# Kernel tuning notes

Measured on AMD Instinct MI355X. Metric: run time of the kernel, lower is better.

## Reference

```python
import jax, jax.numpy as jnp
import numpy as np

N = 8192      # total QM atoms (concatenated over batch)
L = 6         # num_interactions / trajectory length
F = 256       # hidden_size
FH = F // 2
D_RBF = 32    # distance_embedding_size
E = 131072    # total probe edges
P = 32768     # total probes
CUTOFF = 4.0


def silu(x):
    return x * jax.nn.sigmoid(x)


def setup_inputs() -> dict:
    key = jax.random.key(0)
    ks = jax.random.split(key, 20)
    g = lambda k, shp, s=1.0: jax.random.normal(k, shp, dtype=jnp.float32) * s
    s_stack = g(ks[0], (N, L, F))
    v_stack = g(ks[1], (N, L, 3, F))
    # positions in a 2A box so all probe-atom distances < cutoff=4A
    atom_xyz = jax.random.uniform(ks[2], (N, 3), dtype=jnp.float32) * 2.0
    probe_xyz = jax.random.uniform(ks[3], (P, 3), dtype=jnp.float32) * 2.0
    cell = jnp.eye(3, dtype=jnp.float32) * 2.0
    probe_edges_displacement = jnp.zeros((E, 3), dtype=jnp.float32)
    atom_idx = jax.random.randint(ks[4], (E,), 0, N)
    probe_idx = jax.random.randint(ks[5], (E,), 0, P)
    probe_edges = jnp.stack([atom_idx, probe_idx], axis=1)
    in_dim = D_RBF + 3 * F  # e_pi || q_pi || n_i || S_JK
    return {
        's_stack': s_stack,
        'v_stack': v_stack,
        'atom_xyz': atom_xyz,
        'probe_xyz': probe_xyz,
        'cell': cell,
        'probe_edges_displacement': probe_edges_displacement,
        # JK attention MLP: F -> F/2 -> 1
        'attn_w1': g(ks[6], (F, FH), 1.0 / np.sqrt(F)),
        'attn_b1': jnp.zeros((FH,), jnp.float32),
        'attn_w2': g(ks[7], (FH, 1), 1.0 / np.sqrt(FH)),
        'attn_b2': jnp.zeros((1,), jnp.float32),
        # readout msg MLP: (D_rbf+3F) -> F -> F/2 -> 1
        'msg_w1': g(ks[8], (in_dim, F), 1.0 / np.sqrt(in_dim)),
        'msg_b1': jnp.zeros((F,), jnp.float32),
        'msg_w2': g(ks[9], (F, FH), 1.0 / np.sqrt(F)),
        'msg_b2': jnp.zeros((FH,), jnp.float32),
        'msg_w3': g(ks[10], (FH, 1), 1.0 / np.sqrt(FH)),
        'msg_b3': jnp.zeros((1,), jnp.float32),
        'probe_edges': probe_edges,
    }


def reference(s_stack, v_stack, atom_xyz, probe_xyz, cell, probe_edges_displacement,
              attn_w1, attn_b1, attn_w2, attn_b2,
              msg_w1, msg_b1, msg_w2, msg_b2, msg_w3, msg_b3,
              probe_edges):
    # ---- JKNetAggregation: node-level attention over layer trajectory ----
    h = silu(jnp.einsum('nlf,fh->nlh', s_stack, attn_w1) + attn_b1)   # [N,L,F/2]
    logits = (jnp.einsum('nlh,ho->nlo', h, attn_w2) + attn_b2)[..., 0]  # [N,L]
    a = jax.nn.softmax(logits, axis=1)                                  # [N,L]
    S_JK = jnp.einsum('nl,nlf->nf', a, s_stack)                         # [N,F]
    V_JK = jnp.einsum('nl,nlcf->ncf', a, v_stack)                       # [N,3,F]

    # ---- InfoBottleneckReadout: gather -> per-edge MLP -> scatter ----
    atom_idx = probe_edges[:, 0]
    probe_idx = probe_edges[:, 1]
    shift = probe_edges_displacement @ cell                             # [E,3] PBC shift
    diff = probe_xyz[probe_idx] - (atom_xyz[atom_idx] + shift)          # [E,3]
    dist = jnp.linalg.norm(diff, axis=-1)                               # [E]
    d = dist[:, None]
    n = jnp.arange(1, D_RBF + 1, dtype=jnp.float32)
    e_pi = jnp.sin(d * n * jnp.pi / CUTOFF) / (d + 1e-8)                # [E,D_rbf] sinc RBF
    r_hat = diff / (d + 1e-8)                                           # [E,3]
    V_e = V_JK[atom_idx]                                                # [E,3,F]
    q_pi = jnp.einsum('ecf,ec->ef', V_e, r_hat)                         # [E,F]
    n_i = jnp.linalg.norm(V_JK, axis=1)                                 # [N,F]
    h_pi = jnp.concatenate([e_pi, q_pi, n_i[atom_idx], S_JK[atom_idx]], axis=-1)  # [E,D_rbf+3F]
    m = silu(h_pi @ msg_w1 + msg_b1)
    m = silu(m @ msg_w2 + msg_b2)
    m = (m @ msg_w3 + msg_b3)[:, 0]                                     # [E]
    cw = jnp.where(dist < CUTOFF, 0.5 * (jnp.cos(jnp.pi * dist / CUTOFF) + 1.0), 0.0)
    rho = jax.ops.segment_sum(m * cw, probe_idx, num_segments=P)        # [P]
    return rho
```

## Files before the change

kernel.cpp:

```cpp
#include <hip/hip_runtime.h>
#include <math.h>
#include <stdint.h>


#define L_DIM 6
#define F_DIM 256
#define FH_DIM 128
#define DRBF 32
#define CUTOFF_F 4.0f
#define PI_F 3.14159265358979323846f

using bf16x8 = __attribute__((ext_vector_type(8))) short;
using f32x4v = __attribute__((ext_vector_type(4))) float;

__device__ __forceinline__ float silu_f(float x){ return x / (1.f + __expf(-x)); }

__device__ __forceinline__ unsigned short f2bf(float f){
    uint32_t u = __float_as_uint(f);
    uint32_t r = (u + 0x7fffu + ((u >> 16) & 1u)) >> 16;
    return (unsigned short)r;
}

__global__ __launch_bounds__(256) void kPrep(
    const float* __restrict__ msg_w1, const float* __restrict__ msg_w2,
    const float* __restrict__ attn_w1,
    unsigned short* __restrict__ w1bt, unsigned short* __restrict__ w1cdt,
    unsigned short* __restrict__ w2t, unsigned short* __restrict__ wA1t,
    float* __restrict__ rho, int P, int* __restrict__ cntpos, int CN)
{
    int idx = blockIdx.x * 256 + threadIdx.x;
    if (idx < 65536){
        int k = idx >> 8, j = idx & 255;
        w1bt[(size_t)j * 256 + k] = f2bf(msg_w1[(size_t)(DRBF + k) * F_DIM + j]);
    } else if (idx < 196608){
        int i2 = idx - 65536;
        int k = i2 >> 8, j = i2 & 255;
        w1cdt[(size_t)j * 512 + k] = f2bf(msg_w1[(size_t)(DRBF + 256 + k) * F_DIM + j]);
    } else if (idx < 229376){
        int i3 = idx - 196608;
        int k = i3 >> 7, h = i3 & 127;
        w2t[(size_t)h * 256 + k] = f2bf(msg_w2[(size_t)k * FH_DIM + h]);
    } else if (idx < 262144){
        int i4 = idx - 229376;
        int j = i4 >> 8, k = i4 & 255;
        wA1t[(size_t)j * 256 + k] = f2bf(attn_w1[(size_t)k * FH_DIM + j]);
    } else if (idx < 262144 + 32768){
        int i5 = idx - 262144;
        if (i5 < P) rho[i5] = 0.f;
    } else {
        int i6 = idx - 262144 - 32768;
        if (i6 < CN) cntpos[i6] = 0;
    }
}

__global__ __launch_bounds__(256) void kAW(
    const float* __restrict__ s_stack, const float* __restrict__ v_stack,
    const unsigned short* __restrict__ wA1t,
    const float* __restrict__ attn_b1, const float* __restrict__ attn_w2,
    unsigned short* __restrict__ VJKb, unsigned short* __restrict__ NISb,
    const int* __restrict__ pe, int* __restrict__ cnt, int E, int N)
{
    __shared__ float part[4][48];
    __shared__ float aw_l[8][8];

    const int t  = threadIdx.x;
    const int l  = t & 63;
    const int w  = t >> 6;
    const int lm = l & 15, lq = l >> 4;

    bf16x8 bfr[2][8];
    #pragma unroll
    for (int nt2 = 0; nt2 < 2; nt2++){
        const int col = w*32 + nt2*16 + lm;
        #pragma unroll
        for (int kb = 0; kb < 8; kb++)
            bfr[nt2][kb] = *(const bf16x8*)(wA1t + (size_t)col * 256 + kb*32 + lq*8);
    }
    const float b1a = attn_b1[w*32 + lm];
    const float b1b = attn_b1[w*32 + 16 + lm];
    const float w2a = attn_w2[w*32 + lm];
    const float w2b = attn_w2[w*32 + 16 + lm];

    const int n0 = blockIdx.x * 8;
    const size_t rbase = (size_t)n0 * L_DIM;
    const size_t rmax  = (size_t)N * L_DIM - 1;

    #pragma unroll
    for (int mt = 0; mt < 3; mt++){
        const size_t r0 = rbase + mt * 16;
        bf16x8 af[8];
        #pragma unroll
        for (int kb = 0; kb < 8; kb++){
            size_t row = r0 + lm; if (row > rmax) row = rmax;
            const float* ap = s_stack + row * 256 + kb*32 + lq*8;
            float4 fa = *(const float4*)ap;
            float4 fb = *(const float4*)(ap + 4);
            bf16x8 v;
            v[0] = (short)f2bf(fa.x); v[1] = (short)f2bf(fa.y);
            v[2] = (short)f2bf(fa.z); v[3] = (short)f2bf(fa.w);
            v[4] = (short)f2bf(fb.x); v[5] = (short)f2bf(fb.y);
            v[6] = (short)f2bf(fb.z); v[7] = (short)f2bf(fb.w);
            af[kb] = v;
        }
        f32x4v a0 = {0.f,0.f,0.f,0.f}, a1 = {0.f,0.f,0.f,0.f};
        #pragma unroll
        for (int kb = 0; kb < 8; kb++){
            a0 = __builtin_amdgcn_mfma_f32_16x16x32_bf16(af[kb], bfr[0][kb], a0, 0, 0, 0);
            a1 = __builtin_amdgcn_mfma_f32_16x16x32_bf16(af[kb], bfr[1][kb], a1, 0, 0, 0);
        }
        #pragma unroll
        for (int r = 0; r < 4; r++){
            float p = silu_f(a0[r] + b1a) * w2a + silu_f(a1[r] + b1b) * w2b;
            #pragma unroll
            for (int m = 8; m >= 1; m >>= 1) p += __shfl_xor(p, m, 64);
            if (lm == 0) part[w][mt*16 + lq*4 + r] = p;
        }
    }
    __syncthreads();
    if (t < 48) part[0][t] = part[0][t] + part[1][t] + part[2][t] + part[3][t];
    __syncthreads();
    if (t < 8){
        float e[L_DIM]; float mx = -1e30f;
        #pragma unroll
        for (int l6 = 0; l6 < L_DIM; l6++) mx = fmaxf(mx, part[0][t*L_DIM + l6]);
        float s = 0.f;
        #pragma unroll
        for (int l6 = 0; l6 < L_DIM; l6++){ e[l6] = __expf(part[0][t*L_DIM + l6] - mx); s += e[l6]; }
        float inv = 1.f / s;
        #pragma unroll
        for (int l6 = 0; l6 < L_DIM; l6++) aw_l[t][l6] = e[l6] * inv;
    }
    __syncthreads();

    #pragma unroll
    for (int aa = 0; aa < 2; aa++){
        const int n = min(n0 + w*2 + aa, N - 1);
        float aw[L_DIM];
        #pragma unroll
        for (int l6 = 0; l6 < L_DIM; l6++) aw[l6] = aw_l[w*2 + aa][l6];

        const float* sp = s_stack + (size_t)n * (L_DIM * F_DIM) + l * 4;
        const float* vp = v_stack + (size_t)n * (L_DIM * 3 * F_DIM) + l * 4;
        float4 v0 = {0.f,0.f,0.f,0.f}, v1 = {0.f,0.f,0.f,0.f}, v2 = {0.f,0.f,0.f,0.f};
        float4 sj = {0.f,0.f,0.f,0.f};
        #pragma unroll
        for (int l6 = 0; l6 < L_DIM; l6++){
            const float a = aw[l6];
            float4 ss = *(const float4*)(sp + (size_t)l6 * F_DIM);
            float4 x0 = *(const float4*)(vp + (size_t)(l6*3+0) * F_DIM);
            float4 x1 = *(const float4*)(vp + (size_t)(l6*3+1) * F_DIM);
            float4 x2 = *(const float4*)(vp + (size_t)(l6*3+2) * F_DIM);
            v0.x = fmaf(a, x0.x, v0.x); v0.y = fmaf(a, x0.y, v0.y);
            v0.z = fmaf(a, x0.z, v0.z); v0.w = fmaf(a, x0.w, v0.w);
            v1.x = fmaf(a, x1.x, v1.x); v1.y = fmaf(a, x1.y, v1.y);
            v1.z = fmaf(a, x1.z, v1.z); v1.w = fmaf(a, x1.w, v1.w);
            v2.x = fmaf(a, x2.x, v2.x); v2.y = fmaf(a, x2.y, v2.y);
            v2.z = fmaf(a, x2.z, v2.z); v2.w = fmaf(a, x2.w, v2.w);
            sj.x = fmaf(a, ss.x, sj.x); sj.y = fmaf(a, ss.y, sj.y);
            sj.z = fmaf(a, ss.z, sj.z); sj.w = fmaf(a, ss.w, sj.w);
        }
        float4 ni;
        ni.x = sqrtf(v0.x*v0.x + v1.x*v1.x + v2.x*v2.x);
        ni.y = sqrtf(v0.y*v0.y + v1.y*v1.y + v2.y*v2.y);
        ni.z = sqrtf(v0.z*v0.z + v1.z*v1.z + v2.z*v2.z);
        ni.w = sqrtf(v0.w*v0.w + v1.w*v1.w + v2.w*v2.w);

        ushort4 o;
        o = (ushort4){f2bf(v0.x), f2bf(v0.y), f2bf(v0.z), f2bf(v0.w)};
        *(ushort4*)&VJKb[((size_t)n*3 + 0) * F_DIM + l*4] = o;
        o = (ushort4){f2bf(v1.x), f2bf(v1.y), f2bf(v1.z), f2bf(v1.w)};
        *(ushort4*)&VJKb[((size_t)n*3 + 1) * F_DIM + l*4] = o;
        o = (ushort4){f2bf(v2.x), f2bf(v2.y), f2bf(v2.z), f2bf(v2.w)};
        *(ushort4*)&VJKb[((size_t)n*3 + 2) * F_DIM + l*4] = o;
        o = (ushort4){f2bf(ni.x), f2bf(ni.y), f2bf(ni.z), f2bf(ni.w)};
        *(ushort4*)&NISb[(size_t)n * 512 + l*4] = o;
        o = (ushort4){f2bf(sj.x), f2bf(sj.y), f2bf(sj.z), f2bf(sj.w)};
        *(ushort4*)&NISb[(size_t)n * 512 + 256 + l*4] = o;
    }

    {
        int e = blockIdx.x * 128 + t;
        if (t < 128 && e < E) atomicAdd(&cnt[pe[(size_t)e*2]], 1);
    }
}

__global__ __launch_bounds__(256) void kA2(
    const unsigned short* __restrict__ VJKb, const unsigned short* __restrict__ w1bt,
    const unsigned short* __restrict__ NISb, const unsigned short* __restrict__ w1cdt,
    const float* __restrict__ msg_b1, float* __restrict__ UT4,
    const int* __restrict__ pe, const int* __restrict__ offs,
    int* __restrict__ pos, int* __restrict__ perm, int E,
    int gU, int gUT)
{
    const int t  = threadIdx.x;
    const int l  = t & 63;
    const int w  = t >> 6;
    const int lm = l & 15, lq = l >> 4;

    if ((int)blockIdx.x >= gUT){
        int e = (blockIdx.x - gUT) * 256 + t;
        if (e < E){
            int i = pe[(size_t)e*2];
            int slot = atomicAdd(&pos[i], 1);
            perm[offs[i] + slot] = e;
        }
        return;
    }

    if ((int)blockIdx.x < gU){
        bf16x8 bfr[4][8];
        #pragma unroll
        for (int ct = 0; ct < 4; ct++)
            #pragma unroll
            for (int kb = 0; kb < 8; kb++)
                bfr[ct][kb] = *(const bf16x8*)(w1bt + (size_t)(w*64 + ct*16 + lm) * 256 + kb*32 + lq*8);

        const int r00 = blockIdx.x * 128;
        #pragma unroll 1
        for (int mt = 0; mt < 8; mt++){
            const int r0 = r00 + mt * 16;
            bf16x8 af[8];
            #pragma unroll
            for (int kb = 0; kb < 8; kb++)
                af[kb] = *(const bf16x8*)(VJKb + (size_t)(r0 + lm) * 256 + kb*32 + lq*8);
            f32x4v acc[4];
            #pragma unroll
            for (int ct = 0; ct < 4; ct++) acc[ct] = (f32x4v){0.f,0.f,0.f,0.f};
            #pragma unroll
            for (int kb = 0; kb < 8; kb++)
                #pragma unroll
                for (int ct = 0; ct < 4; ct++)
                    acc[ct] = __builtin_amdgcn_mfma_f32_16x16x32_bf16(af[kb], bfr[ct][kb], acc[ct], 0, 0, 0);
            #pragma unroll
            for (int ct = 0; ct < 4; ct++){
                const int col = w*64 + ct*16 + lm;
                #pragma unroll
                for (int r = 0; r < 4; r++){
                    const int row = r0 + lq*4 + r;
                    const int n = row / 3, c = row - n*3;
                    UT4[(((size_t)n << 8) + col) * 4 + c] = acc[ct][r];
                }
            }
        }
    } else {
        const int bid = blockIdx.x - gU;
        const int ch = bid & 1;
        const int bm = bid >> 1;

        bf16x8 bfr[2][16];
        #pragma unroll
        for (int ct = 0; ct < 2; ct++)
            #pragma unroll
            for (int kb = 0; kb < 16; kb++)
                bfr[ct][kb] = *(const bf16x8*)(w1cdt + (size_t)(ch*128 + w*32 + ct*16 + lm) * 512 + kb*32 + lq*8);

        const int r00 = bm * 128;
        #pragma unroll 1
        for (int mt = 0; mt < 8; mt++){
            const int r0 = r00 + mt * 16;
            bf16x8 af[16];
            #pragma unroll
            for (int kb = 0; kb < 16; kb++)
                af[kb] = *(const bf16x8*)(NISb + (size_t)(r0 + lm) * 512 + kb*32 + lq*8);
            f32x4v acc[2];
            #pragma unroll
            for (int ct = 0; ct < 2; ct++) acc[ct] = (f32x4v){0.f,0.f,0.f,0.f};
            #pragma unroll
            for (int kb = 0; kb < 16; kb++)
                #pragma unroll
                for (int ct = 0; ct < 2; ct++)
                    acc[ct] = __builtin_amdgcn_mfma_f32_16x16x32_bf16(af[kb], bfr[ct][kb], acc[ct], 0, 0, 0);
            #pragma unroll
            for (int ct = 0; ct < 2; ct++){
                const int col = ch*128 + w*32 + ct*16 + lm;
                const float bias = msg_b1[col];
                #pragma unroll
                for (int r = 0; r < 4; r++){
                    const int n = r0 + lq*4 + r;
                    UT4[(((size_t)n << 8) + col) * 4 + 3] = acc[ct][r] + bias;
                }
            }
        }
    }
}

__global__ __launch_bounds__(1024) void kScan(const int* __restrict__ cnt, int* __restrict__ off, int N){
    __shared__ int sums[1024];
    const int t = threadIdx.x;
    const int base = t * 8;
    int c[8]; int s = 0;
    #pragma unroll
    for (int j = 0; j < 8; j++){
        int v = (base + j < N) ? cnt[base + j] : 0;
        c[j] = s; s += v;
    }
    sums[t] = s;
    __syncthreads();
    for (int d = 1; d < 1024; d <<= 1){
        int v = (t >= d) ? sums[t - d] : 0;
        __syncthreads();
        sums[t] += v;
        __syncthreads();
    }
    int excl = (t == 0) ? 0 : sums[t - 1];
    #pragma unroll
    for (int j = 0; j < 8; j++)
        if (base + j < N) off[base + j] = excl + c[j];
    if (t == 1023) off[N] = sums[1023];
}

__global__ __launch_bounds__(256) void kB1(
    const int* __restrict__ pe, const float* __restrict__ disp,
    const float* __restrict__ cell,
    const float* __restrict__ atom_xyz, const float* __restrict__ probe_xyz,
    const float* __restrict__ UT4,
    const float* __restrict__ msg_w1,
    const unsigned short* __restrict__ w2t, const float* __restrict__ msg_b2,
    const float* __restrict__ msg_w3, const float* __restrict__ msg_b3,
    const int* __restrict__ perm,
    float* __restrict__ rho, int E)
{
    __shared__ unsigned short x_lds[32 * 256];
    __shared__ unsigned short epi_b[32 * 40];
    __shared__ int   ai_l[32];
    __shared__ int   pp_l[32];
    __shared__ float4 rc4_l[32];
    __shared__ float part[4][32];

    char* xbase = (char*)x_lds;

    const int t  = threadIdx.x;
    const int l  = t & 63;
    const int w  = t >> 6;
    const int lq = l >> 4;
    const int lm = l & 15;

    const float c0 = cell[0], c1 = cell[1], c2 = cell[2];
    const float c3 = cell[3], c4 = cell[4], c5 = cell[5];
    const float c6 = cell[6], c7 = cell[7], c8 = cell[8];

    bf16x8 w1afr[4];
    #pragma unroll
    for (int nt = 0; nt < 4; nt++){
        const int col = w*64 + nt*16 + lm;
        bf16x8 v;
        #pragma unroll
        for (int j = 0; j < 8; j++)
            v[j] = (short)f2bf(msg_w1[(size_t)(lq*8 + j) * F_DIM + col]);
        w1afr[nt] = v;
    }

    bf16x8 bfr[2][8];
    #pragma unroll
    for (int nt2 = 0; nt2 < 2; nt2++){
        const int h = w*32 + nt2*16 + lm;
        #pragma unroll
        for (int kb = 0; kb < 8; kb++)
            bfr[nt2][kb] = *(const bf16x8*)(w2t + (size_t)h * F_DIM + kb*32 + lq*8);
    }
    const float b2v0 = msg_b2[w*32 + lm];
    const float b2v1 = msg_b2[w*32 + 16 + lm];
    const float w3v0 = msg_w3[w*32 + lm];
    const float w3v1 = msg_w3[w*32 + 16 + lm];
    const float b3   = msg_b3[0];

    const int e0 = blockIdx.x * 128;

    int ee_r[4], ia_r[4], ip_r[4];
    #pragma unroll
    for (int bb = 0; bb < 4; bb++){
        int s = min(e0 + bb*32 + (t >> 3), E - 1);
        ee_r[bb] = perm[s];
    }
    #pragma unroll
    for (int bb = 0; bb < 4; bb++){
        ia_r[bb] = pe[(size_t)ee_r[bb]*2];
        ip_r[bb] = pe[(size_t)ee_r[bb]*2 + 1];
    }

    #pragma unroll 1
    for (int bb = 0; bb < 4; bb++){
        const int e0b = e0 + bb * 32;

        {
            const int slot = t >> 3, q = t & 7;
            const int ee = ee_r[bb];
            const int ia = ia_r[bb];
            const int ip = ip_r[bb];
            const float d0 = disp[(size_t)ee*3], d1 = disp[(size_t)ee*3+1], d2 = disp[(size_t)ee*3+2];
            const float sx = d0*c0 + d1*c3 + d2*c6;
            const float sy = d0*c1 + d1*c4 + d2*c7;
            const float sz = d0*c2 + d1*c5 + d2*c8;
            const float dx = probe_xyz[(size_t)ip*3+0] - (atom_xyz[(size_t)ia*3+0] + sx);
            const float dy = probe_xyz[(size_t)ip*3+1] - (atom_xyz[(size_t)ia*3+1] + sy);
            const float dz = probe_xyz[(size_t)ip*3+2] - (atom_xyz[(size_t)ia*3+2] + sz);
            const float dist = sqrtf(dx*dx + dy*dy + dz*dz);
            const float inv  = 1.f / (dist + 1e-8f);
            const float base = dist * (PI_F / CUTOFF_F);
            ushort4 eb;
            eb.x = f2bf(__sinf(base * (float)(q*4 + 1)) * inv);
            eb.y = f2bf(__sinf(base * (float)(q*4 + 2)) * inv);
            eb.z = f2bf(__sinf(base * (float)(q*4 + 3)) * inv);
            eb.w = f2bf(__sinf(base * (float)(q*4 + 4)) * inv);
            *(ushort4*)&epi_b[slot*40 + q*4] = eb;
            if (q == 0){
                ai_l[slot] = ia;
                pp_l[slot] = ip;
                float cw = (dist < CUTOFF_F) ? 0.5f * (__cosf(base) + 1.f) : 0.f;
                rc4_l[slot] = (float4){dx*inv, dy*inv, dz*inv, cw};
            }
        }
        __syncthreads();

        f32x4v pacc[2][4];
        #pragma unroll
        for (int mt = 0; mt < 2; mt++)
            #pragma unroll
            for (int nt = 0; nt < 4; nt++) pacc[mt][nt] = (f32x4v){0.f,0.f,0.f,0.f};
        #pragma unroll
        for (int mt = 0; mt < 2; mt++){
            const bf16x8 af = *(const bf16x8*)&epi_b[(mt*16 + lm)*40 + lq*8];
            #pragma unroll
            for (int nt = 0; nt < 4; nt++)
                pacc[mt][nt] = __builtin_amdgcn_mfma_f32_16x16x32_bf16(af, w1afr[nt], pacc[mt][nt], 0, 0, 0);
        }

        #pragma unroll
        for (int mt = 0; mt < 2; mt++){
            #pragma unroll
            for (int r = 0; r < 4; r++){
                const int e = mt*16 + lq*4 + r;
                const int i = ai_l[e];
                const float4 rc = rc4_l[e];
                const float* up = UT4 + ((size_t)i << 10);
                #pragma unroll
                for (int nt = 0; nt < 4; nt++){
                    const int col = w*64 + nt*16 + lm;
                    const float4 ut = *(const float4*)(up + (size_t)col * 4);
                    float z = pacc[mt][nt][r] + ut.w;
                    z = fmaf(rc.x, ut.x, fmaf(rc.y, ut.y, fmaf(rc.z, ut.z, z)));
                    const int wofs = e*512 + ((col*2) ^ ((e & 7) << 4));
                    *(unsigned short*)(xbase + wofs) = f2bf(silu_f(z));
                }
            }
        }
        __syncthreads();

        f32x4v acc00 = {0.f,0.f,0.f,0.f}, acc01 = {0.f,0.f,0.f,0.f};
        f32x4v acc10 = {0.f,0.f,0.f,0.f}, acc11 = {0.f,0.f,0.f,0.f};
        const int eA0 = lm;
        const int eA1 = 16 + lm;
        #pragma unroll
        for (int kb = 0; kb < 8; kb++){
            const int ko = kb*64 + lq*16;
            bf16x8 af0 = *(const bf16x8*)(xbase + eA0*512 + (ko ^ ((eA0 & 7) << 4)));
            bf16x8 af1 = *(const bf16x8*)(xbase + eA1*512 + (ko ^ ((eA1 & 7) << 4)));
            acc00 = __builtin_amdgcn_mfma_f32_16x16x32_bf16(af0, bfr[0][kb], acc00, 0, 0, 0);
            acc01 = __builtin_amdgcn_mfma_f32_16x16x32_bf16(af0, bfr[1][kb], acc01, 0, 0, 0);
            acc10 = __builtin_amdgcn_mfma_f32_16x16x32_bf16(af1, bfr[0][kb], acc10, 0, 0, 0);
            acc11 = __builtin_amdgcn_mfma_f32_16x16x32_bf16(af1, bfr[1][kb], acc11, 0, 0, 0);
        }

        float pr0[4], pr1[4];
        #pragma unroll
        for (int r = 0; r < 4; r++){
            pr0[r] = silu_f(acc00[r] + b2v0) * w3v0 + silu_f(acc01[r] + b2v1) * w3v1;
            pr1[r] = silu_f(acc10[r] + b2v0) * w3v0 + silu_f(acc11[r] + b2v1) * w3v1;
        }
        #pragma unroll
        for (int r = 0; r < 4; r++){
            #pragma unroll
            for (int m = 8; m >= 1; m >>= 1){
                pr0[r] += __shfl_xor(pr0[r], m, 64);
                pr1[r] += __shfl_xor(pr1[r], m, 64);
            }
        }
        if (lm == 0){
            #pragma unroll
            for (int r = 0; r < 4; r++){
                part[w][lq*4 + r]      = pr0[r];
                part[w][16 + lq*4 + r] = pr1[r];
            }
        }
        __syncthreads();

        if (t < 32 && (e0b + t) < E){
            float tot = part[0][t] + part[1][t] + part[2][t] + part[3][t] + b3;
            atomicAdd(&rho[pp_l[t]], tot * rc4_l[t].w);
        }
        __syncthreads();
    }
}

extern "C" void kernel_launch(void* const* d_in, const int* in_sizes, int n_in,
                              void* d_out, int out_size, void* d_ws, size_t ws_size,
                              hipStream_t stream)
{
    const float* s_stack   = (const float*)d_in[0];
    const float* v_stack   = (const float*)d_in[1];
    const float* atom_xyz  = (const float*)d_in[2];
    const float* probe_xyz = (const float*)d_in[3];
    const float* cell      = (const float*)d_in[4];
    const float* disp      = (const float*)d_in[5];
    const float* attn_w1   = (const float*)d_in[6];
    const float* attn_b1   = (const float*)d_in[7];
    const float* attn_w2   = (const float*)d_in[8];
    const float* msg_w1    = (const float*)d_in[10];
    const float* msg_b1    = (const float*)d_in[11];
    const float* msg_w2    = (const float*)d_in[12];
    const float* msg_b2    = (const float*)d_in[13];
    const float* msg_w3    = (const float*)d_in[14];
    const float* msg_b3    = (const float*)d_in[15];
    const int*   pe        = (const int*)d_in[16];

    const int N = in_sizes[0] / (L_DIM * F_DIM);
    const int E = in_sizes[16] / 2;
    const int P = out_size;
    const size_t NF = (size_t)N * F_DIM;

    float* ws = (float*)d_ws;
    unsigned short* VJKb = (unsigned short*)ws;
    unsigned short* NISb = VJKb + 3*NF;
    float* UT4 = ws + (5*NF)/2;
    unsigned short* w1bt  = (unsigned short*)(ws + (13*NF)/2);
    unsigned short* w1cdt = w1bt + 65536;
    unsigned short* w2t   = w1cdt + 131072;
    unsigned short* wA1t  = w2t + 32768;
    int* cnt  = (int*)(wA1t + 32768);
    int* pos  = cnt + N;
    int* offs = pos + N;
    int* perm = offs + N + 1;

    const int prepElems = 262144 + 32768 + 2 * N;
    kPrep<<<(prepElems + 255) / 256, 256, 0, stream>>>(
        msg_w1, msg_w2, attn_w1, w1bt, w1cdt, w2t, wA1t,
        (float*)d_out, P, cnt, 2 * N);

    kAW<<<(N + 7) / 8, 256, 0, stream>>>(s_stack, v_stack, wA1t, attn_b1, attn_w2,
                                         VJKb, NISb, pe, cnt, E, N);

    kScan<<<1, 1024, 0, stream>>>(cnt, offs, N);

    const int gU  = (3 * N) / 128;
    const int gT  = (N / 128) * 2;
    const int gUT = gU + gT;
    const int gS  = (E + 255) / 256;
    kA2<<<gUT + gS, 256, 0, stream>>>(VJKb, w1bt, NISb, w1cdt, msg_b1, UT4,
                                      pe, offs, pos, perm, E, gU, gUT);

    kB1<<<(E + 127) / 128, 256, 0, stream>>>(pe, disp, cell, atom_xyz, probe_xyz,
                                             UT4, msg_w1,
                                             w2t, msg_b2, msg_w3, msg_b3,
                                             perm, (float*)d_out, E);
}
```

Baseline: 176.3 us.

## Double-buffer per-tile LDS and replace cross-wave reduction with direct atomics

Shared buffers for edge features, x activations and per-edge metadata are double-buffered by tile parity. This lets the two trailing __syncthreads per tile be removed. The cross-wave partial-sum reduction through LDS is replaced by each wave issuing its own atomicAdd into rho, with the output bias added only by wave 0. This removes two block barriers per tile but raises the number of global atomics fourfold. It also relies on double buffering being enough to avoid write-after-read hazards across tiles.

```diff
diff --git a/kernel.cpp b/kernel.cpp
--- a/kernel.cpp
+++ b/kernel.cpp
@@ -320,14 +320,11 @@
     const int* __restrict__ perm,
     float* __restrict__ rho, int E)
 {
-    __shared__ unsigned short x_lds[32 * 256];
-    __shared__ unsigned short epi_b[32 * 40];
-    __shared__ int   ai_l[32];
-    __shared__ int   pp_l[32];
-    __shared__ float4 rc4_l[32];
-    __shared__ float part[4][32];
-
-    char* xbase = (char*)x_lds;
+    __shared__ unsigned short x_lds[2][32 * 256];
+    __shared__ unsigned short epi_b[2][32 * 40];
+    __shared__ int   ai_l[2][32];
+    __shared__ int   pp_l[2][32];
+    __shared__ float4 rc4_l[2][32];
 
     const int t  = threadIdx.x;
     const int l  = t & 63;
@@ -363,6 +360,7 @@
     const float w3v0 = msg_w3[w*32 + lm];
     const float w3v1 = msg_w3[w*32 + 16 + lm];
     const float b3   = msg_b3[0];
+    const float b3w  = (w == 0) ? b3 : 0.f;
 
     const int e0 = blockIdx.x * 128;
 
@@ -381,6 +379,8 @@
     #pragma unroll 1
     for (int bb = 0; bb < 4; bb++){
         const int e0b = e0 + bb * 32;
+        const int par = bb & 1;
+        char* xbase = (char*)x_lds[par];
 
         {
             const int slot = t >> 3, q = t & 7;
@@ -402,12 +402,12 @@
             eb.y = f2bf(__sinf(base * (float)(q*4 + 2)) * inv);
             eb.z = f2bf(__sinf(base * (float)(q*4 + 3)) * inv);
             eb.w = f2bf(__sinf(base * (float)(q*4 + 4)) * inv);
-            *(ushort4*)&epi_b[slot*40 + q*4] = eb;
+            *(ushort4*)&epi_b[par][slot*40 + q*4] = eb;
             if (q == 0){
-                ai_l[slot] = ia;
-                pp_l[slot] = ip;
+                ai_l[par][slot] = ia;
+                pp_l[par][slot] = ip;
                 float cw = (dist < CUTOFF_F) ? 0.5f * (__cosf(base) + 1.f) : 0.f;
-                rc4_l[slot] = (float4){dx*inv, dy*inv, dz*inv, cw};
+                rc4_l[par][slot] = (float4){dx*inv, dy*inv, dz*inv, cw};
             }
         }
         __syncthreads();
@@ -419,7 +419,7 @@
             for (int nt = 0; nt < 4; nt++) pacc[mt][nt] = (f32x4v){0.f,0.f,0.f,0.f};
         #pragma unroll
         for (int mt = 0; mt < 2; mt++){
-            const bf16x8 af = *(const bf16x8*)&epi_b[(mt*16 + lm)*40 + lq*8];
+            const bf16x8 af = *(const bf16x8*)&epi_b[par][(mt*16 + lm)*40 + lq*8];
             #pragma unroll
             for (int nt = 0; nt < 4; nt++)
                 pacc[mt][nt] = __builtin_amdgcn_mfma_f32_16x16x32_bf16(af, w1afr[nt], pacc[mt][nt], 0, 0, 0);
@@ -430,8 +430,8 @@
             #pragma unroll
             for (int r = 0; r < 4; r++){
                 const int e = mt*16 + lq*4 + r;
-                const int i = ai_l[e];
-                const float4 rc = rc4_l[e];
+                const int i = ai_l[par][e];
+                const float4 rc = rc4_l[par][e];
                 const float* up = UT4 + ((size_t)i << 10);
                 #pragma unroll
                 for (int nt = 0; nt < 4; nt++){
@@ -478,17 +478,14 @@
         if (lm == 0){
             #pragma unroll
             for (int r = 0; r < 4; r++){
-                part[w][lq*4 + r]      = pr0[r];
-                part[w][16 + lq*4 + r] = pr1[r];
+                const int s0 = lq*4 + r;
+                const int s1 = 16 + lq*4 + r;
+                if ((e0b + s0) < E)
+                    atomicAdd(&rho[pp_l[par][s0]], (pr0[r] + b3w) * rc4_l[par][s0].w);
+                if ((e0b + s1) < E)
+                    atomicAdd(&rho[pp_l[par][s1]], (pr1[r] + b3w) * rc4_l[par][s1].w);
             }
         }
-        __syncthreads();
-
-        if (t < 32 && (e0b + t) < E){
-            float tot = part[0][t] + part[1][t] + part[2][t] + part[3][t] + b3;
-            atomicAdd(&rho[pp_l[t]], tot * rc4_l[t].w);
-        }
-        __syncthreads();
     }
 }
 
```

Result: slower. 182.5 us (+3.6%).
